# Kernel optimization log

Hardware: AMD Instinct MI355X
Metric: run time of the kernel (lower is better)

## Reference

```python
import jax, jax.numpy as jnp
import numpy as np

NF, LF, D_E, D_R = 32, 9, 200, 200
N_ENT, B = 100000, 1024
EPS = 1e-5


def _bn(x, gamma, beta, axes):
    # training-mode batchnorm: biased variance over `axes`
    m = jnp.mean(x, axis=axes, keepdims=True)
    v = jnp.var(x, axis=axes, keepdims=True)
    return (x - m) * jax.lax.rsqrt(v + EPS) * gamma + beta


def setup_inputs() -> dict:
    key = jax.random.key(0)
    ks = jax.random.split(key, 8)
    fc1_len = NF * LF                      # 288
    fc_len = (D_E - LF + 1) * NF           # 6144
    return {
        "e1": jax.random.normal(ks[0], (B, D_E), jnp.float32),
        "r": jax.random.normal(ks[1], (B, D_R), jnp.float32),
        "fc1_w": jax.random.normal(ks[2], (fc1_len, D_R), jnp.float32) * 0.05,
        "fc1_b": jnp.zeros((fc1_len,), jnp.float32),
        "fc_w": jax.random.normal(ks[3], (D_E, fc_len), jnp.float32) * 0.02,
        "fc_b": jnp.zeros((D_E,), jnp.float32),
        "E": jax.random.normal(ks[4], (N_ENT, D_E), jnp.float32) * 0.05,
        "b": jnp.zeros((N_ENT,), jnp.float32),
        "bn0_g": jnp.ones((1,), jnp.float32),
        "bn0_b": jnp.zeros((1,), jnp.float32),
        "bn1_g": jnp.ones((NF,), jnp.float32),
        "bn1_b": jnp.zeros((NF,), jnp.float32),
        "bn2_g": jnp.ones((D_E,), jnp.float32),
        "bn2_b": jnp.zeros((D_E,), jnp.float32),
    }


def reference(e1, r, fc1_w, fc1_b, fc_w, fc_b, E, b,
              bn0_g, bn0_b, bn1_g, bn1_b, bn2_g, bn2_b):
    L = D_E - LF + 1                       # 192 output positions
    # bn0 over [B,1,d_e]: normalize across batch and length (1 channel)
    x = _bn(e1[:, None, :], bn0_g[None, :, None], bn0_b[None, :, None], (0, 2))
    x = x[:, 0, :]                         # [B, d_e]
    # hypernetwork: per-sample conv filters [B, nf, lf]
    k = (r @ fc1_w.T + fc1_b).reshape(B, NF, LF)
    # grouped conv1d (groups=B) == per-sample sliding-window contraction
    idx = jnp.arange(L)[:, None] + jnp.arange(LF)[None, :]   # [L, lf]
    Xw = x[:, idx]                          # [B, L, lf] windows
    conv = jnp.einsum('blj,bfj->bfl', Xw, k)  # [B, nf, L]
    # bn1 over channels nf
    y = _bn(conv, bn1_g[None, :, None], bn1_b[None, :, None], (0, 2))
    y = y.reshape(B, NF * L)
    y = y @ fc_w.T + fc_b                   # [B, d_e]
    y = _bn(y, bn2_g[None, :], bn2_b[None, :], (0,))
    y = jax.nn.relu(y)
    scores = y @ E.T + b                    # [B, n_ent]
    return jax.nn.sigmoid(scores)
```

## Files before the change

kernel.cpp:

```cpp
#include <hip/hip_runtime.h>
#include <math.h>

#define B_    1024
#define DE    200
#define DR    200
#define NFC   32
#define LFC   9
#define LL    192
#define FC1LEN 288
#define FCLEN 6144
#define NENT  100000
#define EPSI  1e-5f
#define KPAD  224
#define NKS   7
#define YKS   192
#define YSEG  16

#define O_S0    0
#define O_P0    64
#define O_S1    256
#define O_S2    320
#define O_P1    768
#define O_RBF   66304
#define O_W1BF  180992
#define O_K     213248
#define O_CFRAG 508160
#define O_FCWP  3653888
#define O_CVEC  4440320
#define O_PART  4440576
#define O_Y     7717376
#define O_ABF   7922176

typedef __attribute__((ext_vector_type(8))) short bf16x8;
typedef __attribute__((ext_vector_type(4))) float f32x4;

__device__ __forceinline__ float sigm(float x){
  return __fdividef(1.0f, 1.0f + __expf(-x));
}

__device__ __forceinline__ unsigned short f2bf(float f){
  unsigned int u = __float_as_uint(f);
  u = (u + 0x7FFFu + ((u >> 16) & 1u)) >> 16;
  return (unsigned short)u;
}

__device__ __forceinline__ bf16x8 pack8(float4 f0, float4 f1){
  bf16x8 o;
  o[0]=(short)f2bf(f0.x); o[1]=(short)f2bf(f0.y); o[2]=(short)f2bf(f0.z); o[3]=(short)f2bf(f0.w);
  o[4]=(short)f2bf(f1.x); o[5]=(short)f2bf(f1.y); o[6]=(short)f2bf(f1.z); o[7]=(short)f2bf(f1.w);
  return o;
}

__global__ void k_bn0_part(const float* __restrict__ e1, float* __restrict__ ws){
  __shared__ float ss[256], sq[256];
  int tid = threadIdx.x;
  float a = 0.f, b = 0.f;
  for (int i = blockIdx.x*256 + tid; i < B_*DE; i += 64*256){
    float v = e1[i]; a += v; b += v*v;
  }
  ss[tid]=a; sq[tid]=b; __syncthreads();
  for (int s=128; s>0; s>>=1){
    if (tid < s){ ss[tid]+=ss[tid+s]; sq[tid]+=sq[tid+s]; }
    __syncthreads();
  }
  if (tid==0){ ws[O_P0+2*blockIdx.x]=ss[0]; ws[O_P0+2*blockIdx.x+1]=sq[0]; }
}

__global__ void k_bn0_final(const float* __restrict__ g, const float* __restrict__ bt,
                            float* __restrict__ ws){
  int tid = threadIdx.x;
  float a = ws[O_P0+2*tid], b = ws[O_P0+2*tid+1];
  for (int o=32; o>0; o>>=1){ a += __shfl_down(a,o); b += __shfl_down(b,o); }
  if (tid==0){
    float n = (float)(B_*DE);
    float m = a/n, v = b/n - m*m;
    float s = rsqrtf(v + EPSI) * g[0];
    ws[O_S0]   = s;
    ws[O_S0+1] = bt[0] - m*s;
  }
}

__global__ void k_rbf(const float* __restrict__ r, float* __restrict__ ws){
  int s = blockIdx.x*256 + threadIdx.x;
  int lane = s & 63;
  int ks = (s >> 6) % NKS;
  int mtile = (s >> 6) / NKS;
  int m = mtile*16 + (lane & 15);
  int k0 = ks*32 + (lane >> 4)*8;
  unsigned short o8[8];
  #pragma unroll
  for (int j = 0; j < 8; ++j){
    int k = k0 + j;
    o8[j] = f2bf((k < DR) ? r[m*DR + k] : 0.f);
  }
  *(bf16x8*)((unsigned short*)(ws + O_RBF) + (size_t)s*8) = *(bf16x8*)o8;
}

__global__ void k_w1bf(const float* __restrict__ w, float* __restrict__ ws){
  int s = blockIdx.x*256 + threadIdx.x;
  if (s >= 18*NKS*64) return;
  int lane = s & 63;
  int ks = (s >> 6) % NKS;
  int ntile = (s >> 6) / NKS;
  int n = ntile*16 + (lane & 15);
  int k0 = ks*32 + (lane >> 4)*8;
  unsigned short o8[8];
  #pragma unroll
  for (int j = 0; j < 8; ++j){
    int k = k0 + j;
    o8[j] = f2bf((k < DR) ? w[(size_t)n*DR + k] : 0.f);
  }
  *(bf16x8*)((unsigned short*)(ws + O_W1BF) + (size_t)s*8) = *(bf16x8*)o8;
}

__global__ void k_fc1m(const float* __restrict__ bias, float* __restrict__ ws){
  const unsigned short* Rb = (const unsigned short*)(ws + O_RBF);
  const unsigned short* Wb = (const unsigned short*)(ws + O_W1BF);
  int mt = blockIdx.x;
  int nt = blockIdx.y;
  int lane = threadIdx.x;
  int lr = lane & 15, lg = lane >> 4;
  f32x4 acc[4] = {};
  #pragma unroll
  for (int ks = 0; ks < NKS; ++ks){
    bf16x8 b = *(const bf16x8*)(Wb + ((size_t)(nt*NKS + ks)*64 + lane)*8);
    #pragma unroll
    for (int mf = 0; mf < 4; ++mf){
      bf16x8 a = *(const bf16x8*)(Rb + ((size_t)((mt*4+mf)*NKS + ks)*64 + lane)*8);
      acc[mf] = __builtin_amdgcn_mfma_f32_16x16x32_bf16(a, b, acc[mf], 0, 0, 0);
    }
  }
  int col = nt*16 + lr;
  float bv = bias[col];
  #pragma unroll
  for (int mf = 0; mf < 4; ++mf){
    int row = mt*64 + mf*16 + lg*4;
    #pragma unroll
    for (int r = 0; r < 4; ++r)
      ws[O_K + (size_t)(row + r)*FC1LEN + col] = acc[mf][r] + bv;
  }
}

__global__ void k_conv(const float* __restrict__ e1, float* __restrict__ ws){
  __shared__ float xs[DE];
  __shared__ float kf[FC1LEN];
  int b = blockIdx.x, tid = threadIdx.x;
  float s0v = ws[O_S0], t0v = ws[O_S0+1];
  for (int d = tid; d < DE;     d += 256) xs[d] = e1[b*DE + d]*s0v + t0v;
  for (int i = tid; i < FC1LEN; i += 256) kf[i] = ws[O_K + (size_t)b*FC1LEN + i];
  __syncthreads();
  unsigned short* Cf = (unsigned short*)(ws + O_CFRAG);
  int f = tid >> 3, sub = tid & 7;
  int mtile = b >> 4, mlan = b & 15;
  float kr[LFC];
  #pragma unroll
  for (int j = 0; j < LFC; ++j) kr[j] = kf[f*LFC + j];
  float sum = 0.f, sq = 0.f;
  #pragma unroll
  for (int g = 0; g < 3; ++g){
    unsigned short o8[8];
    int l0 = sub*24 + g*8;
    #pragma unroll
    for (int t = 0; t < 8; ++t){
      int l = l0 + t;
      float acc = 0.f;
      #pragma unroll
      for (int j = 0; j < LFC; ++j) acc += xs[l+j]*kr[j];
      o8[t] = f2bf(acc);
      sum += acc; sq += acc*acc;
    }
    int k0 = f*LL + l0;
    int ks = k0 >> 5;
    int lane_w = ((k0 >> 3) & 3)*16 + mlan;
    size_t slot = (size_t)(mtile*YKS + ks)*64 + lane_w;
    *(bf16x8*)(Cf + slot*8) = *(bf16x8*)o8;
  }
  for (int o = 1; o < 8; o <<= 1){ sum += __shfl_xor(sum,o); sq += __shfl_xor(sq,o); }
  if (sub == 0){
    ws[O_P1 + (b*NFC + f)*2    ] = sum;
    ws[O_P1 + (b*NFC + f)*2 + 1] = sq;
  }
}

__global__ void k_bn1_final(const float* __restrict__ g, const float* __restrict__ bt,
                            float* __restrict__ ws){
  __shared__ float ss[256], sq[256];
  int f = blockIdx.x, tid = threadIdx.x;
  float a = 0.f, b = 0.f;
  for (int i = tid; i < B_; i += 256){
    a += ws[O_P1 + (i*NFC + f)*2];
    b += ws[O_P1 + (i*NFC + f)*2 + 1];
  }
  ss[tid]=a; sq[tid]=b; __syncthreads();
  for (int s=128; s>0; s>>=1){
    if (tid < s){ ss[tid]+=ss[tid+s]; sq[tid]+=sq[tid+s]; }
    __syncthreads();
  }
  if (tid==0){
    float n = (float)(B_*LL);
    float m = ss[0]/n, v = sq[0]/n - m*m;
    float s = rsqrtf(v + EPSI) * g[f];
    ws[O_S1 + f]       = s;
    ws[O_S1 + NFC + f] = bt[f] - m*s;
  }
}

__global__ void k_fcwp(const float* __restrict__ fcw, float* __restrict__ ws){
  int s = blockIdx.x*256 + threadIdx.x;
  int lane = s & 63;
  int ks = (s >> 6) % YKS;
  int ntile = (s >> 6) / YKS;
  int n = ntile*16 + (lane & 15);
  int k0 = ks*32 + (lane >> 4)*8;
  int f = (k0 >> 6) / 3;
  float sc = ws[O_S1 + f];
  unsigned short o8[8];
  if (n < DE){
    const float* p = fcw + (size_t)n*FCLEN + k0;
    float4 f0 = *(const float4*)p;
    float4 f1 = *(const float4*)(p + 4);
    o8[0]=f2bf(f0.x*sc); o8[1]=f2bf(f0.y*sc); o8[2]=f2bf(f0.z*sc); o8[3]=f2bf(f0.w*sc);
    o8[4]=f2bf(f1.x*sc); o8[5]=f2bf(f1.y*sc); o8[6]=f2bf(f1.z*sc); o8[7]=f2bf(f1.w*sc);
  } else {
    #pragma unroll
    for (int j = 0; j < 8; ++j) o8[j] = 0;
  }
  *(bf16x8*)((unsigned short*)(ws + O_FCWP) + (size_t)s*8) = *(bf16x8*)o8;
}

__global__ void k_cvec(const float* __restrict__ fcw, const float* __restrict__ fcb,
                       float* __restrict__ ws){
  __shared__ float t1s[NFC];
  __shared__ float red[256];
  int o = blockIdx.x, tid = threadIdx.x;
  if (tid < NFC) t1s[tid] = ws[O_S1 + NFC + tid];
  __syncthreads();
  float acc = 0.f;
  for (int i = tid; i < FCLEN; i += 256)
    acc += fcw[(size_t)o*FCLEN + i] * t1s[i/LL];
  red[tid] = acc; __syncthreads();
  for (int s=128; s>0; s>>=1){
    if (tid < s) red[tid] += red[tid+s];
    __syncthreads();
  }
  if (tid==0) ws[O_CVEC + o] = red[0] + fcb[o];
}

__global__ __launch_bounds__(256) void k_ygemm_m(float* __restrict__ ws){
  const unsigned short* Cb = (const unsigned short*)(ws + O_CFRAG);
  const unsigned short* Wb = (const unsigned short*)(ws + O_FCWP);
  int mt = blockIdx.x;
  int seg = blockIdx.y;
  int tid = threadIdx.x;
  int lane = tid & 63, wid = tid >> 6;
  int lr = lane & 15, lg = lane >> 4;
  f32x4 acc[4][4] = {};
  #pragma unroll 4
  for (int ksl = 0; ksl < 12; ++ksl){
    int ks = seg*12 + ksl;
    bf16x8 a[4], bfr[4];
    #pragma unroll
    for (int mf = 0; mf < 4; ++mf)
      a[mf] = *(const bf16x8*)(Cb + ((size_t)((mt*4+mf)*YKS + ks)*64 + lane)*8);
    #pragma unroll
    for (int nf = 0; nf < 4; ++nf){
      int nt = wid*4 + nf;
      bfr[nf] = *(const bf16x8*)(Wb + ((size_t)(nt*YKS + ks)*64 + lane)*8);
    }
    #pragma unroll
    for (int mf = 0; mf < 4; ++mf)
      #pragma unroll
      for (int nf = 0; nf < 4; ++nf)
        acc[mf][nf] = __builtin_amdgcn_mfma_f32_16x16x32_bf16(a[mf], bfr[nf], acc[mf][nf], 0, 0, 0);
  }
  float* part = ws + O_PART + (size_t)seg*(B_*DE);
  #pragma unroll
  for (int nf = 0; nf < 4; ++nf){
    int col = (wid*4 + nf)*16 + lr;
    if (col < DE){
      #pragma unroll
      for (int mf = 0; mf < 4; ++mf){
        int row = mt*64 + mf*16 + lg*4;
        #pragma unroll
        for (int r = 0; r < 4; ++r)
          part[(size_t)(row + r)*DE + col] = acc[mf][nf][r];
      }
    }
  }
}

__global__ void k_yreduce(float* __restrict__ ws){
  int i = blockIdx.x*256 + threadIdx.x;
  int o = i % DE;
  float y = ws[O_CVEC + o];
  #pragma unroll
  for (int s = 0; s < YSEG; ++s) y += ws[O_PART + (size_t)s*(B_*DE) + i];
  ws[O_Y + i] = y;
}

__global__ void k_bn2(const float* __restrict__ g, const float* __restrict__ bt,
                      float* __restrict__ ws){
  __shared__ float ss[256], sq[256];
  int o = blockIdx.x, tid = threadIdx.x;
  float a = 0.f, b = 0.f;
  for (int i = tid; i < B_; i += 256){
    float v = ws[O_Y + i*DE + o];
    a += v; b += v*v;
  }
  ss[tid]=a; sq[tid]=b; __syncthreads();
  for (int s=128; s>0; s>>=1){
    if (tid < s){ ss[tid]+=ss[tid+s]; sq[tid]+=sq[tid+s]; }
    __syncthreads();
  }
  if (tid==0){
    float n = (float)B_;
    float m = ss[0]/n, v = sq[0]/n - m*m;
    float s = rsqrtf(v + EPSI) * g[o];
    ws[O_S2 + o]      = s;
    ws[O_S2 + DE + o] = bt[o] - m*s;
  }
}

__global__ void k_abf(float* __restrict__ ws){
  int s = blockIdx.x*256 + threadIdx.x;
  int lane = s & 63;
  int ks = (s >> 6) % NKS;
  int mtile = (s >> 6) / NKS;
  int m = mtile*16 + (lane & 15);
  int k0 = ks*32 + (lane >> 4)*8;
  unsigned short o8[8];
  #pragma unroll
  for (int j = 0; j < 8; ++j){
    int k = k0 + j;
    float v = 0.f;
    if (k < DE){
      float y = ws[O_Y + m*DE + k];
      v = fmaxf(y*ws[O_S2 + k] + ws[O_S2 + DE + k], 0.f);
    }
    o8[j] = f2bf(v);
  }
  *(bf16x8*)((unsigned short*)(ws + O_ABF) + (size_t)s*8) = *(bf16x8*)o8;
}

__global__ __launch_bounds__(256, 2) void k_scores(const float* __restrict__ E,
                                                   const float* __restrict__ bias,
                                                   const float* __restrict__ ws,
                                                   float* __restrict__ out){
  const unsigned short* Abf = (const unsigned short*)(ws + O_ABF);
  int orig = blockIdx.x;
  int xcd = orig & 7, pos = orig >> 3;
  int wgid = (xcd < 6) ? xcd*98 + pos : 588 + (xcd - 6)*97 + pos;
  int mh = wgid / 391, ns = wgid - mh*391;
  int tid = threadIdx.x;
  int lane = tid & 63, wid = tid >> 6;
  int lr = lane & 15, lg = lane >> 4;

  bf16x8 ebf[4][7];
  int   colv[4];
  float bv[4];
  #pragma unroll
  for (int nf = 0; nf < 4; ++nf){
    int col = (ns*16 + wid*4 + nf)*16 + lr;
    colv[nf] = col;
    int nc = (col < NENT) ? col : (NENT-1);
    bv[nf] = bias[nc];
    const float* ep = E + (size_t)nc*DE;
    #pragma unroll
    for (int ks = 0; ks < NKS; ++ks){
      int k0 = ks*32 + lg*8;
      if (k0 + 8 <= DE){
        float4 f0 = *(const float4*)(ep + k0);
        float4 f1 = *(const float4*)(ep + k0 + 4);
        ebf[nf][ks] = pack8(f0, f1);
      } else {
        ebf[nf][ks] = (bf16x8){0,0,0,0,0,0,0,0};
      }
    }
  }

  const unsigned short* aBase = Abf + (size_t)(mh*8)*1792*8 + lane*8;
  #pragma unroll 1
  for (int t = 0; t < 8; ++t){
    const unsigned short* ap = aBase + (size_t)t*1792*8;
    bf16x8 aC[4], aN[4];
    #pragma unroll
    for (int mf = 0; mf < 4; ++mf) aC[mf] = *(const bf16x8*)(ap + (size_t)(mf*NKS)*512);
    f32x4 acc[4][4] = {};
    #pragma unroll
    for (int ks = 0; ks < NKS; ++ks){
      if (ks < NKS-1){
        #pragma unroll
        for (int mf = 0; mf < 4; ++mf)
          aN[mf] = *(const bf16x8*)(ap + (size_t)(mf*NKS + ks + 1)*512);
      }
      #pragma unroll
      for (int mf = 0; mf < 4; ++mf)
        #pragma unroll
        for (int nf = 0; nf < 4; ++nf)
          acc[mf][nf] = __builtin_amdgcn_mfma_f32_16x16x32_bf16(aC[mf], ebf[nf][ks], acc[mf][nf], 0, 0, 0);
      #pragma unroll
      for (int mf = 0; mf < 4; ++mf) aC[mf] = aN[mf];
    }
    int row0 = (mh*8 + t)*64 + lg*4;
    #pragma unroll
    for (int nf = 0; nf < 4; ++nf){
      if (colv[nf] < NENT){
        #pragma unroll
        for (int mf = 0; mf < 4; ++mf){
          size_t base = (size_t)(row0 + mf*16)*NENT + colv[nf];
          #pragma unroll
          for (int r = 0; r < 4; ++r)
            __builtin_nontemporal_store(sigm(acc[mf][nf][r] + bv[nf]), &out[base + (size_t)r*NENT]);
        }
      }
    }
  }
}

extern "C" void kernel_launch(void* const* d_in, const int* in_sizes, int n_in,
                              void* d_out, int out_size, void* d_ws, size_t ws_size,
                              hipStream_t stream){
  (void)in_sizes; (void)n_in; (void)out_size; (void)ws_size;
  const float* e1    = (const float*)d_in[0];
  const float* r     = (const float*)d_in[1];
  const float* fc1_w = (const float*)d_in[2];
  const float* fc1_b = (const float*)d_in[3];
  const float* fc_w  = (const float*)d_in[4];
  const float* fc_b  = (const float*)d_in[5];
  const float* E     = (const float*)d_in[6];
  const float* bE    = (const float*)d_in[7];
  const float* g0    = (const float*)d_in[8];
  const float* b0    = (const float*)d_in[9];
  const float* g1    = (const float*)d_in[10];
  const float* b1    = (const float*)d_in[11];
  const float* g2    = (const float*)d_in[12];
  const float* b2    = (const float*)d_in[13];
  float* ws  = (float*)d_ws;
  float* out = (float*)d_out;

  k_bn0_part  <<<64,  256, 0, stream>>>(e1, ws);
  k_bn0_final <<<1,   64,  0, stream>>>(g0, b0, ws);
  k_rbf       <<<112, 256, 0, stream>>>(r, ws);
  k_w1bf      <<<32,  256, 0, stream>>>(fc1_w, ws);
  k_fc1m      <<<dim3(16,18), 64, 0, stream>>>(fc1_b, ws);
  k_conv      <<<1024,256, 0, stream>>>(e1, ws);
  k_bn1_final <<<32,  256, 0, stream>>>(g1, b1, ws);
  k_fcwp      <<<768, 256, 0, stream>>>(fc_w, ws);
  k_cvec      <<<200, 256, 0, stream>>>(fc_w, fc_b, ws);
  k_ygemm_m   <<<dim3(16,16), 256, 0, stream>>>(ws);
  k_yreduce   <<<800, 256, 0, stream>>>(ws);
  k_bn2       <<<200, 256, 0, stream>>>(g2, b2, ws);
  k_abf       <<<112, 256, 0, stream>>>(ws);
  k_scores    <<<782, 256, 0, stream>>>(E, bE, ws, out);
}
```

Baseline: 231.5 us.

## Stage score tiles in LDS for coalesced vector stores; merge pack kernels

The scores kernel now writes each 64x256 sigmoid tile into shared memory and then stores it with contiguous float4 nontemporal stores per row, instead of scattered 4-byte stores along columns. The XCD-aware block remapping is removed and columns are regrouped into 256-wide contiguous spans per block. The two bf16 packing kernels are merged into one launch. The 64 KB LDS tile and two barriers per iteration may lower occupancy below the declared two blocks per CU.

```diff
diff --git a/kernel.cpp b/kernel.cpp
--- a/kernel.cpp
+++ b/kernel.cpp
@@ -80,37 +80,39 @@
   }
 }
 
-__global__ void k_rbf(const float* __restrict__ r, float* __restrict__ ws){
-  int s = blockIdx.x*256 + threadIdx.x;
-  int lane = s & 63;
-  int ks = (s >> 6) % NKS;
-  int mtile = (s >> 6) / NKS;
-  int m = mtile*16 + (lane & 15);
-  int k0 = ks*32 + (lane >> 4)*8;
-  unsigned short o8[8];
-  #pragma unroll
-  for (int j = 0; j < 8; ++j){
-    int k = k0 + j;
-    o8[j] = f2bf((k < DR) ? r[m*DR + k] : 0.f);
-  }
-  *(bf16x8*)((unsigned short*)(ws + O_RBF) + (size_t)s*8) = *(bf16x8*)o8;
-}
-
-__global__ void k_w1bf(const float* __restrict__ w, float* __restrict__ ws){
-  int s = blockIdx.x*256 + threadIdx.x;
-  if (s >= 18*NKS*64) return;
-  int lane = s & 63;
-  int ks = (s >> 6) % NKS;
-  int ntile = (s >> 6) / NKS;
-  int n = ntile*16 + (lane & 15);
-  int k0 = ks*32 + (lane >> 4)*8;
-  unsigned short o8[8];
-  #pragma unroll
-  for (int j = 0; j < 8; ++j){
-    int k = k0 + j;
-    o8[j] = f2bf((k < DR) ? w[(size_t)n*DR + k] : 0.f);
-  }
-  *(bf16x8*)((unsigned short*)(ws + O_W1BF) + (size_t)s*8) = *(bf16x8*)o8;
+__global__ void k_pack(const float* __restrict__ r, const float* __restrict__ w,
+                       float* __restrict__ ws){
+  int blk = blockIdx.x;
+  if (blk < 112){
+    int s = blk*256 + threadIdx.x;
+    int lane = s & 63;
+    int ks = (s >> 6) % NKS;
+    int mtile = (s >> 6) / NKS;
+    int m = mtile*16 + (lane & 15);
+    int k0 = ks*32 + (lane >> 4)*8;
+    unsigned short o8[8];
+    #pragma unroll
+    for (int j = 0; j < 8; ++j){
+      int k = k0 + j;
+      o8[j] = f2bf((k < DR) ? r[m*DR + k] : 0.f);
+    }
+    *(bf16x8*)((unsigned short*)(ws + O_RBF) + (size_t)s*8) = *(bf16x8*)o8;
+  } else {
+    int s = (blk-112)*256 + threadIdx.x;
+    if (s >= 18*NKS*64) return;
+    int lane = s & 63;
+    int ks = (s >> 6) % NKS;
+    int ntile = (s >> 6) / NKS;
+    int n = ntile*16 + (lane & 15);
+    int k0 = ks*32 + (lane >> 4)*8;
+    unsigned short o8[8];
+    #pragma unroll
+    for (int j = 0; j < 8; ++j){
+      int k = k0 + j;
+      o8[j] = f2bf((k < DR) ? w[(size_t)n*DR + k] : 0.f);
+    }
+    *(bf16x8*)((unsigned short*)(ws + O_W1BF) + (size_t)s*8) = *(bf16x8*)o8;
+  }
 }
 
 __global__ void k_fc1m(const float* __restrict__ bias, float* __restrict__ ws){
@@ -346,22 +348,19 @@
                                                    const float* __restrict__ bias,
                                                    const float* __restrict__ ws,
                                                    float* __restrict__ out){
+  __shared__ float tile[64*256];
   const unsigned short* Abf = (const unsigned short*)(ws + O_ABF);
-  int orig = blockIdx.x;
-  int xcd = orig & 7, pos = orig >> 3;
-  int wgid = (xcd < 6) ? xcd*98 + pos : 588 + (xcd - 6)*97 + pos;
+  int wgid = blockIdx.x;
   int mh = wgid / 391, ns = wgid - mh*391;
   int tid = threadIdx.x;
   int lane = tid & 63, wid = tid >> 6;
   int lr = lane & 15, lg = lane >> 4;
 
   bf16x8 ebf[4][7];
-  int   colv[4];
   float bv[4];
   #pragma unroll
   for (int nf = 0; nf < 4; ++nf){
-    int col = (ns*16 + wid*4 + nf)*16 + lr;
-    colv[nf] = col;
+    int col = ns*256 + wid*64 + nf*16 + lr;
     int nc = (col < NENT) ? col : (NENT-1);
     bv[nf] = bias[nc];
     const float* ep = E + (size_t)nc*DE;
@@ -379,6 +378,7 @@
   }
 
   const unsigned short* aBase = Abf + (size_t)(mh*8)*1792*8 + lane*8;
+  int col0 = ns*256;
   #pragma unroll 1
   for (int t = 0; t < 8; ++t){
     const unsigned short* ap = aBase + (size_t)t*1792*8;
@@ -401,18 +401,27 @@
       #pragma unroll
       for (int mf = 0; mf < 4; ++mf) aC[mf] = aN[mf];
     }
-    int row0 = (mh*8 + t)*64 + lg*4;
-    #pragma unroll
-    for (int nf = 0; nf < 4; ++nf){
-      if (colv[nf] < NENT){
+    __syncthreads();
+    #pragma unroll
+    for (int mf = 0; mf < 4; ++mf)
+      #pragma unroll
+      for (int nf = 0; nf < 4; ++nf){
+        int lrow = mf*16 + lg*4;
+        int lcol = wid*64 + nf*16 + lr;
         #pragma unroll
-        for (int mf = 0; mf < 4; ++mf){
-          size_t base = (size_t)(row0 + mf*16)*NENT + colv[nf];
-          #pragma unroll
-          for (int r = 0; r < 4; ++r)
-            __builtin_nontemporal_store(sigm(acc[mf][nf][r] + bv[nf]), &out[base + (size_t)r*NENT]);
-        }
+        for (int r = 0; r < 4; ++r)
+          tile[(lrow + r)*256 + lcol] = sigm(acc[mf][nf][r] + bv[nf]);
       }
+    __syncthreads();
+    int row0 = (mh*8 + t)*64;
+    #pragma unroll
+    for (int p = 0; p < 16; ++p){
+      int lrow = p*4 + wid;
+      int lcol = lane*4;
+      f32x4 v = *(const f32x4*)&tile[lrow*256 + lcol];
+      int gc = col0 + lcol;
+      if (gc < NENT)
+        __builtin_nontemporal_store(v, (f32x4*)&out[(size_t)(row0 + lrow)*NENT + gc]);
     }
   }
 }
@@ -440,8 +449,7 @@
 
   k_bn0_part  <<<64,  256, 0, stream>>>(e1, ws);
   k_bn0_final <<<1,   64,  0, stream>>>(g0, b0, ws);
-  k_rbf       <<<112, 256, 0, stream>>>(r, ws);
-  k_w1bf      <<<32,  256, 0, stream>>>(fc1_w, ws);
+  k_pack      <<<144, 256, 0, stream>>>(r, fc1_w, ws);
   k_fc1m      <<<dim3(16,18), 64, 0, stream>>>(fc1_b, ws);
   k_conv      <<<1024,256, 0, stream>>>(e1, ws);
   k_bn1_final <<<32,  256, 0, stream>>>(g1, b1, ws);
```

Result: faster. 200.9 us (-13.2%).
